# Performance work log

Hardware: AMD Instinct MI355X
Metric: run time of the kernel (lower is better)

The kernel has to match this reference:

```python
import jax, jax.numpy as jnp
import numpy as np


def pam(x, Wb, bb, Wc, bc, Wd, bd, alpha):
    # x: [B, C, h, w] ; 1x1 convs are channel matmuls
    B, C, h, w = x.shape
    L = h * w
    xf = x.reshape(B, C, L)                                   # [B,C,L]
    fb = jnp.einsum('oc,bcl->bol', Wb, xf) + bb[None, :, None]  # [B,C8,L]
    fc = jnp.einsum('oc,bcl->bol', Wc, xf) + bc[None, :, None]  # [B,C8,L]
    fd = jnp.einsum('oc,bcl->bol', Wd, xf) + bd[None, :, None]  # [B,C,L]
    # attention_s = softmax(feat_b^T @ feat_c) over last dim: [B,L,L]
    attn = jax.nn.softmax(jnp.einsum('bol,bom->blm', fb, fc), axis=-1)
    # feat_e = feat_d @ attn^T : [B,C,L]
    fe = jnp.einsum('bcm,blm->bcl', fd, attn)
    out = alpha * fe + xf
    return out.reshape(B, C, h, w)


def light_pam(x, Wb1, bb1, Wc1, bc1, Wd1, bd1, alpha1,
              Wb2, bb2, Wc2, bc2, Wd2, bd2, alpha2, P_h, P_w):
    N, C, H, W = x.shape
    Q_h, Q_w = H // P_h, W // P_w
    x = x.reshape(N, C, Q_h, P_h, Q_w, P_w)
    x = x.transpose(0, 3, 5, 1, 2, 4).reshape(N * P_h * P_w, C, Q_h, Q_w)
    x = pam(x, Wb1, bb1, Wc1, bc1, Wd1, bd1, alpha1)
    x = x.reshape(N, P_h, P_w, C, Q_h, Q_w)
    x = x.transpose(0, 4, 5, 3, 1, 2).reshape(N * Q_h * Q_w, C, P_h, P_w)
    x = pam(x, Wb2, bb2, Wc2, bc2, Wd2, bd2, alpha2)
    x = x.reshape(N, Q_h, Q_w, C, P_h, P_w)
    return x.transpose(0, 3, 1, 4, 2, 5).reshape(N, C, H, W)


def setup_inputs() -> dict:
    key = jax.random.key(0)
    ks = jax.random.split(key, 9)
    C, C8 = 256, 32
    s = 0.05
    return {
        'x': jax.random.normal(ks[0], (8, C, 128, 128), jnp.float32),
        'Wb1': jax.random.normal(ks[1], (C8, C), jnp.float32) * s,
        'bb1': jnp.zeros((C8,), jnp.float32),
        'Wc1': jax.random.normal(ks[2], (C8, C), jnp.float32) * s,
        'bc1': jnp.zeros((C8,), jnp.float32),
        'Wd1': jax.random.normal(ks[3], (C, C), jnp.float32) * s,
        'bd1': jnp.zeros((C,), jnp.float32),
        'alpha1': jnp.zeros((1,), jnp.float32),
        'Wb2': jax.random.normal(ks[4], (C8, C), jnp.float32) * s,
        'bb2': jnp.zeros((C8,), jnp.float32),
        'Wc2': jax.random.normal(ks[5], (C8, C), jnp.float32) * s,
        'bc2': jnp.zeros((C8,), jnp.float32),
        'Wd2': jax.random.normal(ks[6], (C, C), jnp.float32) * s,
        'bd2': jnp.zeros((C,), jnp.float32),
        'alpha2': jax.random.normal(ks[7], (1,), jnp.float32) * 0.1,
    }


def reference(x, Wb1, bb1, Wc1, bc1, Wd1, bd1, alpha1,
              Wb2, bb2, Wc2, bc2, Wd2, bd2, alpha2):
    return light_pam(x, Wb1, bb1, Wc1, bc1, Wd1, bd1, alpha1,
                     Wb2, bb2, Wc2, bc2, Wd2, bd2, alpha2, 8, 8)
```

## Files before the change

### kernel.cpp

```cpp
#include <hip/hip_runtime.h>
#include <stdint.h>

typedef unsigned int u32;
typedef unsigned short u16;

#define C_   256
#define C8_  32
#define H_   128
#define W_   128
#define HW_  (H_*W_)

typedef __bf16 bf16x8_t __attribute__((ext_vector_type(8)));
typedef float  f32x4_t  __attribute__((ext_vector_type(4)));

__device__ __forceinline__ float bf2f(u32 u) {
    union { u32 i; float f; } v; v.i = u << 16; return v.f;
}
__device__ __forceinline__ u16 f2bf(float f) {
    union { float f; u32 i; } v; v.f = f;
    u32 r = v.i + 0x7fffu + ((v.i >> 16) & 1u);
    return (u16)(r >> 16);
}
__device__ __forceinline__ bf16x8_t ld_frag(const u16* p) {
    union { uint4 u; bf16x8_t b; } x; x.u = *(const uint4*)p; return x.b;
}

#define WS_XF1   0
#define WS_XF2   67108864
#define WS_WBC2  134217728
#define WS_WD2   (134217728+32768)
#define WS_GEN   134479872
#define WS_FB1   WS_GEN
#define WS_FC1   (WS_GEN + 16777216)
#define WS_FD1   (WS_GEN + 33554432)

__global__ __launch_bounds__(256) void k_wpack(
    const float* __restrict__ Wb2, const float* __restrict__ Wc2,
    const float* __restrict__ Wd2, u16* __restrict__ Wbc2, u16* __restrict__ Wd2b)
{
    int gid = blockIdx.x * 256 + threadIdx.x;
    if (gid < 16384) {
        int o = gid >> 8, c = gid & 255;
        float v = (o < 32) ? Wb2[o*256 + c] : Wc2[(o-32)*256 + c];
        Wbc2[gid] = f2bf(v);
    } else if (gid < 81920) {
        Wd2b[gid - 16384] = f2bf(Wd2[gid - 16384]);
    }
}

__global__ __launch_bounds__(256) void k_gather(
    const float* __restrict__ x, const float* __restrict__ alpha1,
    u16* __restrict__ xf1, u16* __restrict__ xf2)
{
    __shared__ __align__(16) u16 xt[128 * 130];
    int id = blockIdx.x;
    int n = id >> 8, h = (id >> 1) & 127, ch = id & 1;
    int qh = h >> 3, ph = h & 7;
    const float* xb = x + (((size_t)(n*256 + ch*128)) * 128 + h) * 128;
    #pragma unroll
    for (int s = 0; s < 16; ++s) {
        int idx = threadIdx.x + 256 * s;
        int cc = idx >> 5, w4 = idx & 31;
        float4 v = *(const float4*)(xb + (size_t)cc * HW_ + w4 * 4);
        u32 p0 = (u32)f2bf(v.x) | ((u32)f2bf(v.y) << 16);
        u32 p1 = (u32)f2bf(v.z) | ((u32)f2bf(v.w) << 16);
        ((u32*)xt)[cc * 65 + w4 * 2]     = p0;
        ((u32*)xt)[cc * 65 + w4 * 2 + 1] = p1;
    }
    __syncthreads();
    int t = threadIdx.x;
    int r = t & 127, seg = t >> 7;
    int qw = r >> 3, pw = r & 7;
    int wcol = qw * 8 + pw;
    u32 buf[32];
    #pragma unroll
    for (int k = 0; k < 32; ++k) {
        u16 a = xt[(seg * 64 + 2 * k)     * 130 + wcol];
        u16 b = xt[(seg * 64 + 2 * k + 1) * 130 + wcol];
        buf[k] = (u32)a | ((u32)b << 16);
    }
    size_t b1 = (size_t)n * 64 + ph * 8 + pw;
    size_t l1 = qh * 16 + qw;
    u32* d1 = (u32*)(xf1 + (b1 * 256 + l1) * 256 + ch * 128 + seg * 64);
    #pragma unroll
    for (int k = 0; k < 32; ++k) d1[k] = buf[k];
    if (alpha1[0] == 0.f) {
        size_t b2 = (size_t)n * 256 + qh * 16 + qw;
        size_t l2 = ph * 8 + pw;
        u32* d2 = (u32*)(xf2 + (b2 * 64 + l2) * 256 + ch * 128 + seg * 64);
        #pragma unroll
        for (int k = 0; k < 32; ++k) d2[k] = buf[k];
    }
}

__global__ __launch_bounds__(256) void k_fbfc1(
    const float* __restrict__ x, const float* __restrict__ Wb,
    const float* __restrict__ bb, const float* __restrict__ Wc,
    const float* __restrict__ bc, float* __restrict__ fb, float* __restrict__ fc,
    const float* __restrict__ alpha)
{
    if (alpha[0] == 0.f) return;
    __shared__ __align__(16) float xt[C_ * 32];
    const int tile = blockIdx.x;
    const int b = blockIdx.y;
    const int t = threadIdx.x;
    const int n = b >> 6, ph = (b >> 3) & 7, pw = b & 7;
    const float* xb = x + (size_t)n * C_ * HW_;
    #pragma unroll
    for (int s = 0; s < 32; ++s) {
        int i = t + 256 * s;
        int c = i >> 5, l = i & 31;
        int l1 = tile * 32 + l;
        int qh = l1 >> 4, qw = l1 & 15;
        xt[c * 32 + l] = xb[(size_t)c * HW_ + (qh * 8 + ph) * W_ + (qw * 8 + pw)];
    }
    __syncthreads();
    const int l = t & 31;
    const int og = t >> 5;
    const float* Wp = (og < 4) ? Wb : Wc;
    const float* bp = (og < 4) ? bb : bc;
    float* op = (og < 4) ? fb : fc;
    const int ob = (og & 3) * 8;
    float acc[8];
    #pragma unroll
    for (int j = 0; j < 8; ++j) acc[j] = bp[ob + j];
    for (int c = 0; c < C_; ++c) {
        float xv = xt[c * 32 + l];
        #pragma unroll
        for (int j = 0; j < 8; ++j)
            acc[j] += Wp[(ob + j) * C_ + c] * xv;
    }
    #pragma unroll
    for (int j = 0; j < 8; ++j)
        op[((size_t)b * C8_ + ob + j) * 256 + tile * 32 + l] = acc[j];
}

__global__ __launch_bounds__(256) void k_fd1(
    const float* __restrict__ x, const float* __restrict__ Wd,
    const float* __restrict__ bd, u16* __restrict__ fd,
    const float* __restrict__ alpha)
{
    if (alpha[0] == 0.f) return;
    __shared__ __align__(16) float xt[C_ * 32];
    const int tile = blockIdx.x, b = blockIdx.y, t = threadIdx.x;
    const int n = b >> 6, ph = (b >> 3) & 7, pw = b & 7;
    const float* xb = x + (size_t)n * C_ * HW_;
    #pragma unroll
    for (int s = 0; s < 32; ++s) {
        int i = t + 256 * s;
        int k = i >> 5, m = i & 31;
        int l1 = tile * 32 + m;
        int qh = l1 >> 4, qw = l1 & 15;
        xt[k * 32 + m] = xb[(size_t)k * HW_ + (qh * 8 + ph) * W_ + (qw * 8 + pw)];
    }
    __syncthreads();
    const int c = t;
    float acc[32];
    #pragma unroll
    for (int m = 0; m < 32; ++m) acc[m] = 0.f;
    const float* wrow = Wd + c * C_;
    for (int k = 0; k < C_; k += 4) {
        float4 w = *(const float4*)(wrow + k);
        float wk[4] = {w.x, w.y, w.z, w.w};
        #pragma unroll
        for (int kk = 0; kk < 4; ++kk) {
            const float4* xr = (const float4*)(xt + (k + kk) * 32);
            float wv = wk[kk];
            #pragma unroll
            for (int q = 0; q < 8; ++q) {
                float4 xv = xr[q];
                acc[q*4+0] += wv * xv.x;
                acc[q*4+1] += wv * xv.y;
                acc[q*4+2] += wv * xv.z;
                acc[q*4+3] += wv * xv.w;
            }
        }
    }
    const float bdv = bd[c];
    u32* dst = (u32*)(fd + ((size_t)b * C_ + c) * 256 + tile * 32);
    #pragma unroll
    for (int m = 0; m < 16; ++m) {
        u32 lo = f2bf(acc[2*m] + bdv);
        u32 hi = f2bf(acc[2*m+1] + bdv);
        dst[m] = lo | (hi << 16);
    }
}

__global__ __launch_bounds__(256) void k_attn_fe1(
    const float* __restrict__ x, const float* __restrict__ fb,
    const float* __restrict__ fc, const u16* __restrict__ fd,
    const float* __restrict__ alpha, u16* __restrict__ xf2)
{
    if (alpha[0] == 0.f) return;
    __shared__ __align__(16) float smem[12800];
    float* fbt = smem;
    float* fct = smem + 512;
    float* S   = smem + 8704;
    float* attnT = smem + 512;
    const int tile = blockIdx.x;
    const int b = blockIdx.y, t = threadIdx.x;
    #pragma unroll
    for (int s = 0; s < 2; ++s) {
        int j = t + 256 * s;
        int o = j >> 4, l = j & 15;
        fbt[o * 16 + l] = fb[((size_t)b * C8_ + o) * 256 + tile * 16 + l];
    }
    #pragma unroll
    for (int s = 0; s < 32; ++s) {
        int j = t + 256 * s;
        int o = j >> 8, m = j & 255;
        fct[o * 256 + m] = fc[((size_t)b * C8_ + o) * 256 + m];
    }
    __syncthreads();
    {
        const int lane = t & 63, wv = t >> 6;
        float acc[4][4];
        #pragma unroll
        for (int i = 0; i < 4; ++i)
            #pragma unroll
            for (int j = 0; j < 4; ++j) acc[i][j] = 0.f;
        for (int o = 0; o < 32; ++o) {
            float cv[4];
            #pragma unroll
            for (int j = 0; j < 4; ++j) cv[j] = fct[o * 256 + lane + 64 * j];
            #pragma unroll
            for (int i = 0; i < 4; ++i) {
                float a = fbt[o * 16 + wv * 4 + i];
                #pragma unroll
                for (int j = 0; j < 4; ++j) acc[i][j] += a * cv[j];
            }
        }
        #pragma unroll
        for (int i = 0; i < 4; ++i)
            #pragma unroll
            for (int j = 0; j < 4; ++j)
                S[(wv * 4 + i) * 256 + lane + 64 * j] = acc[i][j];
    }
    __syncthreads();
    {
        const int r = t >> 4, k = t & 15;
        float vals[16];
        float mx = -1e30f;
        #pragma unroll
        for (int j = 0; j < 16; ++j) {
            vals[j] = S[r * 256 + k + 16 * j];
            mx = fmaxf(mx, vals[j]);
        }
        mx = fmaxf(mx, __shfl_xor(mx, 1, 16));
        mx = fmaxf(mx, __shfl_xor(mx, 2, 16));
        mx = fmaxf(mx, __shfl_xor(mx, 4, 16));
        mx = fmaxf(mx, __shfl_xor(mx, 8, 16));
        float sum = 0.f;
        #pragma unroll
        for (int j = 0; j < 16; ++j) { vals[j] = __expf(vals[j] - mx); sum += vals[j]; }
        sum += __shfl_xor(sum, 1, 16);
        sum += __shfl_xor(sum, 2, 16);
        sum += __shfl_xor(sum, 4, 16);
        sum += __shfl_xor(sum, 8, 16);
        const float inv = 1.0f / sum;
        #pragma unroll
        for (int j = 0; j < 16; ++j)
            attnT[(k + 16 * j) * 16 + r] = vals[j] * inv;
    }
    __syncthreads();
    const int c = t;
    float acc[16];
    #pragma unroll
    for (int i = 0; i < 16; ++i) acc[i] = 0.f;
    const u16* fdrow = fd + ((size_t)b * C_ + c) * 256;
    for (int m = 0; m < 256; m += 4) {
        uint2 p = *(const uint2*)(fdrow + m);
        float wm[4] = { bf2f(p.x & 0xffffu), bf2f(p.x >> 16),
                        bf2f(p.y & 0xffffu), bf2f(p.y >> 16) };
        #pragma unroll
        for (int mm = 0; mm < 4; ++mm) {
            const float4* ar = (const float4*)(attnT + (m + mm) * 16);
            float wv = wm[mm];
            #pragma unroll
            for (int q = 0; q < 4; ++q) {
                float4 av = ar[q];
                acc[q*4+0] += wv * av.x;
                acc[q*4+1] += wv * av.y;
                acc[q*4+2] += wv * av.z;
                acc[q*4+3] += wv * av.w;
            }
        }
    }
    const float al = alpha[0];
    const int n = b >> 6, ph = (b >> 3) & 7, pw = b & 7;
    const int l2 = ph * 8 + pw;
    const float* xb = x + (size_t)n * C_ * HW_ + (size_t)c * HW_;
    #pragma unroll
    for (int i = 0; i < 16; ++i) {
        int l1 = tile * 16 + i;
        int qh = l1 >> 4, qw = l1 & 15;
        float xv = xb[(qh * 8 + ph) * W_ + (qw * 8 + pw)];
        size_t b2 = (size_t)n * 256 + qh * 16 + qw;
        xf2[(b2 * 64 + l2) * 256 + c] = f2bf(al * acc[i] + xv);
    }
}

#define FDSLAB 0
#define FBCT   18432
#define ATTN   23040

__global__ __launch_bounds__(256) void k_pam2_fused(
    const u16* __restrict__ xf2, const u16* __restrict__ Wbc2,
    const u16* __restrict__ Wd2, const float* __restrict__ bb2,
    const float* __restrict__ bc2, const float* __restrict__ bd2,
    const float* __restrict__ alpha2, float* __restrict__ out)
{
    __shared__ __align__(16) u16 lds[27648];
    const int b2 = blockIdx.x;
    const int n = b2 >> 8, qh = (b2 >> 4) & 15, qw = b2 & 15;
    const int t = threadIdx.x;
    const int w = t >> 6, lane = t & 63;
    const int q = lane >> 4, i = lane & 15;
    const int ls = w * 16;
    const u16* xrow0 = xf2 + (size_t)b2 * 64 * 256;

    f32x4_t acc1[4];
    #pragma unroll
    for (int mt = 0; mt < 4; ++mt) acc1[mt] = (f32x4_t){0.f,0.f,0.f,0.f};
    for (int ks = 0; ks < 8; ++ks) {
        int kb = ks * 32 + q * 8;
        bf16x8_t bfr = ld_frag(xrow0 + (size_t)(ls + i) * 256 + kb);
        #pragma unroll
        for (int mt = 0; mt < 4; ++mt) {
            bf16x8_t afr = ld_frag(Wbc2 + (mt * 16 + i) * 256 + kb);
            acc1[mt] = __builtin_amdgcn_mfma_f32_16x16x32_bf16(afr, bfr, acc1[mt], 0, 0, 0);
        }
    }
    #pragma unroll
    for (int mt = 0; mt < 4; ++mt) {
        #pragma unroll
        for (int r = 0; r < 4; ++r) {
            int o = mt * 16 + q * 4 + r;
            float bv = (o < 32) ? bb2[o] : bc2[o - 32];
            lds[FBCT + (ls + i) * 72 + o] = f2bf(acc1[mt][r] + bv);
        }
    }
    __syncthreads();

    f32x4_t accS[4];
    #pragma unroll
    for (int nt = 0; nt < 4; ++nt) accS[nt] = (f32x4_t){0.f,0.f,0.f,0.f};
    {
        bf16x8_t afr = ld_frag(&lds[FBCT + (ls + i) * 72 + q * 8]);
        #pragma unroll
        for (int nt = 0; nt < 4; ++nt) {
            bf16x8_t bfr = ld_frag(&lds[FBCT + (nt * 16 + i) * 72 + 32 + q * 8]);
            accS[nt] = __builtin_amdgcn_mfma_f32_16x16x32_bf16(afr, bfr, accS[nt], 0, 0, 0);
        }
    }
    #pragma unroll
    for (int r = 0; r < 4; ++r) {
        int l = ls + q * 4 + r;
        float mx = accS[0][r];
        #pragma unroll
        for (int nt = 1; nt < 4; ++nt) mx = fmaxf(mx, accS[nt][r]);
        mx = fmaxf(mx, __shfl_xor(mx, 1));
        mx = fmaxf(mx, __shfl_xor(mx, 2));
        mx = fmaxf(mx, __shfl_xor(mx, 4));
        mx = fmaxf(mx, __shfl_xor(mx, 8));
        float e[4], sum = 0.f;
        #pragma unroll
        for (int nt = 0; nt < 4; ++nt) { e[nt] = __expf(accS[nt][r] - mx); sum += e[nt]; }
        sum += __shfl_xor(sum, 1);
        sum += __shfl_xor(sum, 2);
        sum += __shfl_xor(sum, 4);
        sum += __shfl_xor(sum, 8);
        float inv = 1.0f / sum;
        #pragma unroll
        for (int nt = 0; nt < 4; ++nt)
            lds[ATTN + l * 72 + nt * 16 + i] = f2bf(e[nt] * inv);
    }

    {
        const int cs = w * 64;
        f32x4_t acc2[4][4];
        #pragma unroll
        for (int mt = 0; mt < 4; ++mt)
            #pragma unroll
            for (int nt = 0; nt < 4; ++nt) acc2[mt][nt] = (f32x4_t){0.f,0.f,0.f,0.f};
        for (int ks = 0; ks < 8; ++ks) {
            int kb = ks * 32 + q * 8;
            bf16x8_t bfr[4];
            #pragma unroll
            for (int nt = 0; nt < 4; ++nt)
                bfr[nt] = ld_frag(xrow0 + (size_t)(nt * 16 + i) * 256 + kb);
            #pragma unroll
            for (int mt = 0; mt < 4; ++mt) {
                bf16x8_t afr = ld_frag(Wd2 + (size_t)(cs + mt * 16 + i) * 256 + kb);
                #pragma unroll
                for (int nt = 0; nt < 4; ++nt)
                    acc2[mt][nt] = __builtin_amdgcn_mfma_f32_16x16x32_bf16(afr, bfr[nt], acc2[mt][nt], 0, 0, 0);
            }
        }
        #pragma unroll
        for (int mt = 0; mt < 4; ++mt) {
            #pragma unroll
            for (int r = 0; r < 4; ++r) {
                int c = cs + mt * 16 + q * 4 + r;
                float bv = bd2[c];
                #pragma unroll
                for (int nt = 0; nt < 4; ++nt)
                    lds[FDSLAB + c * 72 + nt * 16 + i] = f2bf(acc2[mt][nt][r] + bv);
            }
        }
    }
    __syncthreads();

    f32x4_t accE[16];
    #pragma unroll
    for (int nt = 0; nt < 16; ++nt) accE[nt] = (f32x4_t){0.f,0.f,0.f,0.f};
    #pragma unroll
    for (int ks = 0; ks < 2; ++ks) {
        int kb = ks * 32 + q * 8;
        bf16x8_t afr = ld_frag(&lds[ATTN + (ls + i) * 72 + kb]);
        #pragma unroll
        for (int nt = 0; nt < 16; ++nt) {
            bf16x8_t bfr = ld_frag(&lds[FDSLAB + (nt * 16 + i) * 72 + kb]);
            accE[nt] = __builtin_amdgcn_mfma_f32_16x16x32_bf16(afr, bfr, accE[nt], 0, 0, 0);
        }
    }

    const float al = alpha2[0];
    float vals[64];
    #pragma unroll
    for (int nt = 0; nt < 16; ++nt) {
        #pragma unroll
        for (int r = 0; r < 4; ++r) {
            int l = ls + q * 4 + r;
            int c = nt * 16 + i;
            float xv = bf2f(xrow0[(size_t)l * 256 + c]);
            vals[nt * 4 + r] = al * accE[nt][r] + xv;
        }
    }
    float* stg = (float*)lds;
    for (int h = 0; h < 2; ++h) {
        __syncthreads();
        #pragma unroll
        for (int nt = h * 8; nt < h * 8 + 8; ++nt) {
            #pragma unroll
            for (int r = 0; r < 4; ++r) {
                int l = ls + q * 4 + r;
                int cc = nt * 16 + i - h * 128;
                stg[l * 133 + cc] = vals[nt * 4 + r];
            }
        }
        __syncthreads();
        int ph = lane >> 3, pw = lane & 7;
        for (int j = 0; j < 32; ++j) {
            int c = h * 128 + w * 32 + j;
            float v = stg[lane * 133 + (c - h * 128)];
            out[(((size_t)n * 256 + c) * 128 + qh * 8 + ph) * 128 + qw * 8 + pw] = v;
        }
    }
}

extern "C" void kernel_launch(void* const* d_in, const int* in_sizes, int n_in,
                              void* d_out, int out_size, void* d_ws, size_t ws_size,
                              hipStream_t stream)
{
    const float* x   = (const float*)d_in[0];
    const float* Wb1 = (const float*)d_in[1];
    const float* bb1 = (const float*)d_in[2];
    const float* Wc1 = (const float*)d_in[3];
    const float* bc1 = (const float*)d_in[4];
    const float* Wd1 = (const float*)d_in[5];
    const float* bd1 = (const float*)d_in[6];
    const float* a1  = (const float*)d_in[7];
    const float* Wb2 = (const float*)d_in[8];
    const float* bb2 = (const float*)d_in[9];
    const float* Wc2 = (const float*)d_in[10];
    const float* bc2 = (const float*)d_in[11];
    const float* Wd2 = (const float*)d_in[12];
    const float* bd2 = (const float*)d_in[13];
    const float* a2  = (const float*)d_in[14];
    (void)in_sizes; (void)n_in; (void)out_size; (void)ws_size;

    char* ws = (char*)d_ws;
    u16*   xf1  = (u16*)(ws + WS_XF1);
    u16*   xf2  = (u16*)(ws + WS_XF2);
    u16*   Wbc2 = (u16*)(ws + WS_WBC2);
    u16*   Wd2b = (u16*)(ws + WS_WD2);
    float* fb1  = (float*)(ws + WS_FB1);
    float* fc1  = (float*)(ws + WS_FC1);
    u16*   fd1  = (u16*)(ws + WS_FD1);
    float* out  = (float*)d_out;

    k_wpack<<<dim3(320), 256, 0, stream>>>(Wb2, Wc2, Wd2, Wbc2, Wd2b);
    k_gather<<<dim3(2048), 256, 0, stream>>>(x, a1, xf1, xf2);
    k_fbfc1<<<dim3(8, 512), 256, 0, stream>>>(x, Wb1, bb1, Wc1, bc1, fb1, fc1, a1);
    k_fd1<<<dim3(8, 512), 256, 0, stream>>>(x, Wd1, bd1, fd1, a1);
    k_attn_fe1<<<dim3(16, 512), 256, 0, stream>>>(x, fb1, fc1, fd1, a1, xf2);
    k_pam2_fused<<<dim3(2048), 256, 0, stream>>>(xf2, Wbc2, Wd2b, bb2, bc2, bd2, a2, out);
}
```

Baseline: 413.1 us.

## Drop dead xf1 staging, vectorize gather stores, and shrink PAM2 LDS footprint

The gather kernel stops writing the bf16 xf1 buffer, which no later kernel reads, and now always writes xf2 using 16-byte stores and a wider global load pattern. k_attn_fe1 still overwrites xf2 when alpha1 is nonzero. In the fused PAM2 kernel, the fb/fc transposed tile is aliased with the fd slab, which needs an extra barrier and shrinks shared memory so more blocks can be resident. The residual add is moved from the register phase into the final store loop. The main saving is a large unneeded global write, at the cost of one more sync and a changed access pattern for the residual reads.

```diff
diff --git a/kernel.cpp b/kernel.cpp
--- a/kernel.cpp
+++ b/kernel.cpp
@@ -25,11 +25,10 @@
     union { uint4 u; bf16x8_t b; } x; x.u = *(const uint4*)p; return x.b;
 }
 
-#define WS_XF1   0
-#define WS_XF2   67108864
-#define WS_WBC2  134217728
-#define WS_WD2   (134217728+32768)
-#define WS_GEN   134479872
+#define WS_XF2   0
+#define WS_WBC2  67108864
+#define WS_WD2   (67108864+32768)
+#define WS_GEN   (67108864+262144)
 #define WS_FB1   WS_GEN
 #define WS_FC1   (WS_GEN + 16777216)
 #define WS_FD1   (WS_GEN + 33554432)
@@ -49,48 +48,48 @@
 }
 
 __global__ __launch_bounds__(256) void k_gather(
-    const float* __restrict__ x, const float* __restrict__ alpha1,
-    u16* __restrict__ xf1, u16* __restrict__ xf2)
-{
-    __shared__ __align__(16) u16 xt[128 * 130];
-    int id = blockIdx.x;
-    int n = id >> 8, h = (id >> 1) & 127, ch = id & 1;
-    int qh = h >> 3, ph = h & 7;
-    const float* xb = x + (((size_t)(n*256 + ch*128)) * 128 + h) * 128;
-    #pragma unroll
-    for (int s = 0; s < 16; ++s) {
-        int idx = threadIdx.x + 256 * s;
-        int cc = idx >> 5, w4 = idx & 31;
-        float4 v = *(const float4*)(xb + (size_t)cc * HW_ + w4 * 4);
-        u32 p0 = (u32)f2bf(v.x) | ((u32)f2bf(v.y) << 16);
-        u32 p1 = (u32)f2bf(v.z) | ((u32)f2bf(v.w) << 16);
-        ((u32*)xt)[cc * 65 + w4 * 2]     = p0;
-        ((u32*)xt)[cc * 65 + w4 * 2 + 1] = p1;
-    }
-    __syncthreads();
-    int t = threadIdx.x;
-    int r = t & 127, seg = t >> 7;
-    int qw = r >> 3, pw = r & 7;
-    int wcol = qw * 8 + pw;
-    u32 buf[32];
+    const float* __restrict__ x, u16* __restrict__ xf2)
+{
+    __shared__ __align__(16) u16 xt[128 * 132];
+    const int id = blockIdx.x;
+    const int n = id >> 8, h = (id >> 1) & 127, ch = id & 1;
+    const int qh = h >> 3, ph = h & 7;
+    const int t = threadIdx.x;
+    const float* xb = x + ((size_t)(n * 256 + ch * 128)) * HW_ + h * 128;
+    #pragma unroll
+    for (int s = 0; s < 8; ++s) {
+        int idx = t + 256 * s;
+        int c = idx >> 4, wq = idx & 15;
+        const float* p = xb + (size_t)c * HW_ + wq * 8;
+        float4 a = *(const float4*)p;
+        float4 b = *(const float4*)(p + 4);
+        uint2 pk;
+        pk.x = (u32)f2bf(a.x) | ((u32)f2bf(a.y) << 16);
+        pk.y = (u32)f2bf(a.z) | ((u32)f2bf(a.w) << 16);
+        uint2 pk2;
+        pk2.x = (u32)f2bf(b.x) | ((u32)f2bf(b.y) << 16);
+        pk2.y = (u32)f2bf(b.z) | ((u32)f2bf(b.w) << 16);
+        u16* q = xt + c * 132 + wq * 8;
+        *(uint2*)q = pk;
+        *(uint2*)(q + 4) = pk2;
+    }
+    __syncthreads();
+    const int r = t >> 1;
+    const int half = t & 1;
+    const int qw = r >> 3, pw = r & 7;
+    uint4 vbuf[8];
+    u32* buf = (u32*)vbuf;
     #pragma unroll
     for (int k = 0; k < 32; ++k) {
-        u16 a = xt[(seg * 64 + 2 * k)     * 130 + wcol];
-        u16 b = xt[(seg * 64 + 2 * k + 1) * 130 + wcol];
+        u16 a = xt[(half * 64 + 2 * k)     * 132 + r];
+        u16 b = xt[(half * 64 + 2 * k + 1) * 132 + r];
         buf[k] = (u32)a | ((u32)b << 16);
     }
-    size_t b1 = (size_t)n * 64 + ph * 8 + pw;
-    size_t l1 = qh * 16 + qw;
-    u32* d1 = (u32*)(xf1 + (b1 * 256 + l1) * 256 + ch * 128 + seg * 64);
-    #pragma unroll
-    for (int k = 0; k < 32; ++k) d1[k] = buf[k];
-    if (alpha1[0] == 0.f) {
-        size_t b2 = (size_t)n * 256 + qh * 16 + qw;
-        size_t l2 = ph * 8 + pw;
-        u32* d2 = (u32*)(xf2 + (b2 * 64 + l2) * 256 + ch * 128 + seg * 64);
-        #pragma unroll
-        for (int k = 0; k < 32; ++k) d2[k] = buf[k];
-    }
+    size_t b2 = (size_t)n * 256 + qh * 16 + qw;
+    size_t l2 = ph * 8 + pw;
+    uint4* dst = (uint4*)(xf2 + (b2 * 64 + l2) * 256 + ch * 128 + half * 64);
+    #pragma unroll
+    for (int k = 0; k < 8; ++k) dst[k] = vbuf[k];
 }
 
 __global__ __launch_bounds__(256) void k_fbfc1(
@@ -300,9 +299,9 @@
     }
 }
 
+#define FBCT   0
 #define FDSLAB 0
-#define FBCT   18432
-#define ATTN   23040
+#define ATTN   18432
 
 __global__ __launch_bounds__(256) void k_pam2_fused(
     const u16* __restrict__ xf2, const u16* __restrict__ Wbc2,
@@ -310,7 +309,7 @@
     const float* __restrict__ bc2, const float* __restrict__ bd2,
     const float* __restrict__ alpha2, float* __restrict__ out)
 {
-    __shared__ __align__(16) u16 lds[27648];
+    __shared__ __align__(16) u16 lds[23040];
     const int b2 = blockIdx.x;
     const int n = b2 >> 8, qh = (b2 >> 4) & 15, qw = b2 & 15;
     const int t = threadIdx.x;
@@ -375,6 +374,7 @@
         for (int nt = 0; nt < 4; ++nt)
             lds[ATTN + l * 72 + nt * 16 + i] = f2bf(e[nt] * inv);
     }
+    __syncthreads();
 
     {
         const int cs = w * 64;
@@ -430,12 +430,8 @@
     #pragma unroll
     for (int nt = 0; nt < 16; ++nt) {
         #pragma unroll
-        for (int r = 0; r < 4; ++r) {
-            int l = ls + q * 4 + r;
-            int c = nt * 16 + i;
-            float xv = bf2f(xrow0[(size_t)l * 256 + c]);
-            vals[nt * 4 + r] = al * accE[nt][r] + xv;
-        }
+        for (int r = 0; r < 4; ++r)
+            vals[nt * 4 + r] = al * accE[nt][r];
     }
     float* stg = (float*)lds;
     for (int h = 0; h < 2; ++h) {
@@ -453,7 +449,8 @@
         int ph = lane >> 3, pw = lane & 7;
         for (int j = 0; j < 32; ++j) {
             int c = h * 128 + w * 32 + j;
-            float v = stg[lane * 133 + (c - h * 128)];
+            float v = stg[lane * 133 + (c - h * 128)]
+                      + bf2f(xrow0[(size_t)lane * 256 + c]);
             out[(((size_t)n * 256 + c) * 128 + qh * 8 + ph) * 128 + qw * 8 + pw] = v;
         }
     }
@@ -481,7 +478,6 @@
     (void)in_sizes; (void)n_in; (void)out_size; (void)ws_size;
 
     char* ws = (char*)d_ws;
-    u16*   xf1  = (u16*)(ws + WS_XF1);
     u16*   xf2  = (u16*)(ws + WS_XF2);
     u16*   Wbc2 = (u16*)(ws + WS_WBC2);
     u16*   Wd2b = (u16*)(ws + WS_WD2);
@@ -491,7 +487,7 @@
     float* out  = (float*)d_out;
 
     k_wpack<<<dim3(320), 256, 0, stream>>>(Wb2, Wc2, Wd2, Wbc2, Wd2b);
-    k_gather<<<dim3(2048), 256, 0, stream>>>(x, a1, xf1, xf2);
+    k_gather<<<dim3(2048), 256, 0, stream>>>(x, xf2);
     k_fbfc1<<<dim3(8, 512), 256, 0, stream>>>(x, Wb1, bb1, Wc1, bc1, fb1, fc1, a1);
     k_fd1<<<dim3(8, 512), 256, 0, stream>>>(x, Wd1, bd1, fd1, a1);
     k_attn_fe1<<<dim3(16, 512), 256, 0, stream>>>(x, fb1, fc1, fd1, a1, xf2);
```

Result: no change. 414.8 us (+0.4%).
